# Performance work log

Hardware: AMD Instinct MI355X
Metric: run time of the kernel (lower is better)

The kernel has to match this reference:

```python
import jax, jax.numpy as jnp
import numpy as np

NUM_EMBEDDINGS = 1024
EMBEDDING_DIM = 64


def setup_inputs() -> dict:
    key = jax.random.key(0)
    k1, k2 = jax.random.split(key)
    x = jax.random.normal(k1, (32, 64, 32, 32), dtype=jnp.float32)
    # embeddings initialized uniform(-1/K, 1/K) as in the torch module
    codebook = jax.random.uniform(
        k2, (NUM_EMBEDDINGS, EMBEDDING_DIM), dtype=jnp.float32,
        minval=-1.0 / NUM_EMBEDDINGS, maxval=1.0 / NUM_EMBEDDINGS)
    return {"x": x, "codebook": codebook}


def reference(x, codebook):
    # x: [B, D, H, W] -> [B, H, W, D]
    xp = jnp.transpose(x, (0, 2, 3, 1))
    B, H, W, D = xp.shape
    K = codebook.shape[0]
    xf = xp.reshape(-1, D)  # [N, D]
    # squared L2 distances via expansion (argmin identical to torch.norm argmin)
    x2 = jnp.sum(xf * xf, axis=1, keepdims=True)          # [N, 1]
    c2 = jnp.sum(codebook * codebook, axis=1)             # [K]
    d2 = x2 - 2.0 * (xf @ codebook.T) + c2[None, :]       # [N, K]
    idx = jnp.argmin(d2, axis=1)                          # [N]
    encodings = jax.nn.one_hot(idx, K, dtype=jnp.float32)  # [N, K]
    quantized = codebook[idx]                             # [N, D] == encodings @ codebook
    quantized = quantized.reshape(B, H, W, D).transpose(0, 3, 1, 2)
    return encodings, quantized
```

## Files before the change

### kernel.cpp

```cpp
#include <hip/hip_runtime.h>

#define N_PIX   32768
#define DIM     64
#define K_CODES 1024
#define NCHUNK  4
#define CHUNK   (K_CODES / NCHUNK)


__global__ __launch_bounds__(256) void c2_kernel(const float* __restrict__ cb,
                                                 float* __restrict__ c2) {
    int k = blockIdx.x * 256 + threadIdx.x;
    if (k >= K_CODES) return;
    const float* row = cb + k * DIM;
    float a0 = 0.f, a1 = 0.f, a2 = 0.f, a3 = 0.f;
#pragma unroll
    for (int d = 0; d < DIM; d += 4) {
        a0 = fmaf(row[d + 0], row[d + 0], a0);
        a1 = fmaf(row[d + 1], row[d + 1], a1);
        a2 = fmaf(row[d + 2], row[d + 2], a2);
        a3 = fmaf(row[d + 3], row[d + 3], a3);
    }
    c2[k] = (a0 + a1) + (a2 + a3);
}

__global__ __launch_bounds__(256, 2) void argmin_lds(const float* __restrict__ x,
                                                     const float* __restrict__ cb,
                                                     const float* __restrict__ c2,
                                                     float2* __restrict__ part) {
    __shared__ alignas(16) float4 lds_cb[CHUNK * (DIM / 4)];
    __shared__ float lds_c2[CHUNK];

    int blk    = blockIdx.x;
    int pixblk = blk >> 2;
    int chunk  = blk & 3;
    int t  = threadIdx.x;
    int k0 = chunk * CHUNK;

    {
        const float4* cb4 = reinterpret_cast<const float4*>(cb) + (size_t)k0 * (DIM / 4);
#pragma unroll
        for (int i = 0; i < 16; ++i)
            lds_cb[t + i * 256] = cb4[t + i * 256];
        lds_c2[t] = c2[k0 + t];
    }

    int p  = pixblk * 256 + t;
    int bb = p >> 10;
    int hw = p & 1023;

    const float* xb = x + (size_t)bb * (DIM * 1024) + hw;
#define LDX(i) make_float4(xb[(size_t)(4*(i)+0) << 10], xb[(size_t)(4*(i)+1) << 10], \
                           xb[(size_t)(4*(i)+2) << 10], xb[(size_t)(4*(i)+3) << 10])
    float4 x0 = LDX(0),  x1 = LDX(1),  x2v = LDX(2),  x3 = LDX(3);
    float4 x4 = LDX(4),  x5 = LDX(5),  x6 = LDX(6),   x7 = LDX(7);
    float4 x8 = LDX(8),  x9 = LDX(9),  x10 = LDX(10), x11 = LDX(11);
    float4 x12 = LDX(12), x13 = LDX(13), x14 = LDX(14), x15 = LDX(15);
#undef LDX

    float s0 = 0.f, s1 = 0.f, s2 = 0.f, s3 = 0.f;
#define SQ(v) { s0 = fmaf(v.x, v.x, s0); s1 = fmaf(v.y, v.y, s1); \
                s2 = fmaf(v.z, v.z, s2); s3 = fmaf(v.w, v.w, s3); }
    SQ(x0) SQ(x1) SQ(x2v) SQ(x3) SQ(x4) SQ(x5) SQ(x6) SQ(x7)
    SQ(x8) SQ(x9) SQ(x10) SQ(x11) SQ(x12) SQ(x13) SQ(x14) SQ(x15)
#undef SQ
    float x2 = (s0 + s1) + (s2 + s3);

    __syncthreads();

#define PIN(v) asm volatile("" : "+v"(v.x), "+v"(v.y), "+v"(v.z), "+v"(v.w));
    PIN(x0) PIN(x1) PIN(x2v) PIN(x3) PIN(x4) PIN(x5) PIN(x6) PIN(x7)
    PIN(x8) PIN(x9) PIN(x10) PIN(x11) PIN(x12) PIN(x13) PIN(x14) PIN(x15)
#undef PIN

    float best = 1e30f;
    int   bidx = 0;
    for (int kk = 0; kk < CHUNK; ++kk) {
        const float4* wrow = &lds_cb[kk * (DIM / 4)];
        float c2k = lds_c2[kk];
        float a0 = 0.f, a1 = 0.f, a2 = 0.f, a3 = 0.f;
#define STEP(i, xi) { float4 w = wrow[i]; \
        a0 = fmaf(xi.x, w.x, a0); a1 = fmaf(xi.y, w.y, a1); \
        a2 = fmaf(xi.z, w.z, a2); a3 = fmaf(xi.w, w.w, a3); }
        STEP(0, x0)  STEP(1, x1)  STEP(2, x2v)  STEP(3, x3)
        STEP(4, x4)  STEP(5, x5)  STEP(6, x6)   STEP(7, x7)
        STEP(8, x8)  STEP(9, x9)  STEP(10, x10) STEP(11, x11)
        STEP(12, x12) STEP(13, x13) STEP(14, x14) STEP(15, x15)
#undef STEP
        float dot = (a0 + a1) + (a2 + a3);
        float u    = x2 - 2.0f * dot;
        float dist = u + c2k;
        if (dist < best) { best = dist; bidx = k0 + kk; }
    }
    float2 r;
    r.x = best;
    r.y = __int_as_float(bidx);
    part[(size_t)chunk * N_PIX + p] = r;
}

__global__ __launch_bounds__(128) void reduce_quant(const float* __restrict__ cb,
                                                    const float2* __restrict__ part,
                                                    int* __restrict__ idx,
                                                    float* __restrict__ quant) {
    int n = blockIdx.x * 128 + threadIdx.x;
    float best = 1e30f;
    int   bi = 0;
#pragma unroll
    for (int c = 0; c < NCHUNK; ++c) {
        float2 r = part[(size_t)c * N_PIX + n];
        if (r.x < best) { best = r.x; bi = __float_as_int(r.y); }
    }
    idx[n] = bi;

    int bb = n >> 10;
    int hw = n & 1023;
    const float4* crow = reinterpret_cast<const float4*>(cb + (size_t)bi * DIM);
    float* qb = quant + (size_t)bb * (DIM * 1024) + hw;
#pragma unroll
    for (int dq = 0; dq < 16; ++dq) {
        float4 cv = crow[dq];
        qb[(size_t)(dq * 4 + 0) << 10] = cv.x;
        qb[(size_t)(dq * 4 + 1) << 10] = cv.y;
        qb[(size_t)(dq * 4 + 2) << 10] = cv.z;
        qb[(size_t)(dq * 4 + 3) << 10] = cv.w;
    }
}

__global__ __launch_bounds__(256) void enc_write(const int* __restrict__ idx,
                                                 float* __restrict__ enc) {
    const int TOT = (N_PIX / 4) * K_CODES;
    int tid = blockIdx.x * 256 + threadIdx.x;
    float4* enc4 = reinterpret_cast<float4*>(enc);
    for (int e = tid; e < TOT; e += 2048 * 256) {
        int n  = e >> 8;
        int j0 = (e & 255) << 2;
        int ir = idx[n];
        float4 v;
        v.x = (ir == j0 + 0) ? 1.0f : 0.0f;
        v.y = (ir == j0 + 1) ? 1.0f : 0.0f;
        v.z = (ir == j0 + 2) ? 1.0f : 0.0f;
        v.w = (ir == j0 + 3) ? 1.0f : 0.0f;
        enc4[e] = v;
    }
}

extern "C" void kernel_launch(void* const* d_in, const int* in_sizes, int n_in,
                              void* d_out, int out_size, void* d_ws, size_t ws_size,
                              hipStream_t stream) {
    const float* x  = (const float*)d_in[0];
    const float* cb = (const float*)d_in[1];

    float*  c2   = (float*)d_ws;
    float2* part = (float2*)((char*)d_ws + 4096);
    int*    idx  = (int*)((char*)d_ws + 4096 + (size_t)NCHUNK * N_PIX * 8);

    float* enc   = (float*)d_out;
    float* quant = (float*)d_out + (size_t)N_PIX * K_CODES;

    c2_kernel<<<K_CODES / 256, 256, 0, stream>>>(cb, c2);
    argmin_lds<<<(N_PIX / 256) * NCHUNK, 256, 0, stream>>>(x, cb, c2, part);
    reduce_quant<<<N_PIX / 128, 128, 0, stream>>>(cb, part, idx, quant);
    enc_write<<<2048, 256, 0, stream>>>(idx, enc);
}
```

Baseline: 255.4 us.

## Register-block four pixels per thread in argmin and split codebook into eight chunks

Each thread now holds four pixels' 64-dim vectors in registers, so every codebook row read from LDS is reused across four dot products instead of one. To keep the grid size up, the codebook is split into eight chunks of 128 codes rather than four, and the grid becomes 32 pixel blocks times 8 chunks. This cuts LDS read traffic per FMA, but needs about 256 VGPRs for the x values plus accumulators, so launch bounds drop to one block per CU. That risks lower occupancy or spills, and the partial-results buffer and reduce kernel now handle twice as many chunks.

```diff
diff --git a/kernel.cpp b/kernel.cpp
--- a/kernel.cpp
+++ b/kernel.cpp
@@ -3,7 +3,7 @@
 #define N_PIX   32768
 #define DIM     64
 #define K_CODES 1024
-#define NCHUNK  4
+#define NCHUNK  8
 #define CHUNK   (K_CODES / NCHUNK)
 
 
@@ -23,7 +23,7 @@
     c2[k] = (a0 + a1) + (a2 + a3);
 }
 
-__global__ __launch_bounds__(256, 2) void argmin_lds(const float* __restrict__ x,
+__global__ __launch_bounds__(256, 1) void argmin_lds(const float* __restrict__ x,
                                                      const float* __restrict__ cb,
                                                      const float* __restrict__ c2,
                                                      float2* __restrict__ part) {
@@ -31,70 +31,103 @@
     __shared__ float lds_c2[CHUNK];
 
     int blk    = blockIdx.x;
-    int pixblk = blk >> 2;
-    int chunk  = blk & 3;
+    int pixblk = blk >> 3;
+    int chunk  = blk & 7;
     int t  = threadIdx.x;
     int k0 = chunk * CHUNK;
 
     {
         const float4* cb4 = reinterpret_cast<const float4*>(cb) + (size_t)k0 * (DIM / 4);
 #pragma unroll
-        for (int i = 0; i < 16; ++i)
+        for (int i = 0; i < 8; ++i)
             lds_cb[t + i * 256] = cb4[t + i * 256];
-        lds_c2[t] = c2[k0 + t];
+        if (t < CHUNK) lds_c2[t] = c2[k0 + t];
     }
 
-    int p  = pixblk * 256 + t;
-    int bb = p >> 10;
-    int hw = p & 1023;
+    const float* xb0 = x + (size_t)pixblk * (DIM * 1024) + t;
+    const float* xb1 = xb0 + 256;
+    const float* xb2 = xb0 + 512;
+    const float* xb3 = xb0 + 768;
 
-    const float* xb = x + (size_t)bb * (DIM * 1024) + hw;
-#define LDX(i) make_float4(xb[(size_t)(4*(i)+0) << 10], xb[(size_t)(4*(i)+1) << 10], \
-                           xb[(size_t)(4*(i)+2) << 10], xb[(size_t)(4*(i)+3) << 10])
-    float4 x0 = LDX(0),  x1 = LDX(1),  x2v = LDX(2),  x3 = LDX(3);
-    float4 x4 = LDX(4),  x5 = LDX(5),  x6 = LDX(6),   x7 = LDX(7);
-    float4 x8 = LDX(8),  x9 = LDX(9),  x10 = LDX(10), x11 = LDX(11);
-    float4 x12 = LDX(12), x13 = LDX(13), x14 = LDX(14), x15 = LDX(15);
+#define LDX(b, i) make_float4(b[(size_t)(4*(i)+0) << 10], b[(size_t)(4*(i)+1) << 10], \
+                              b[(size_t)(4*(i)+2) << 10], b[(size_t)(4*(i)+3) << 10])
+#define DECLX(p, b) \
+    float4 x##p##_0 = LDX(b,0),  x##p##_1 = LDX(b,1),  x##p##_2 = LDX(b,2),  x##p##_3 = LDX(b,3), \
+           x##p##_4 = LDX(b,4),  x##p##_5 = LDX(b,5),  x##p##_6 = LDX(b,6),  x##p##_7 = LDX(b,7), \
+           x##p##_8 = LDX(b,8),  x##p##_9 = LDX(b,9),  x##p##_10 = LDX(b,10), x##p##_11 = LDX(b,11), \
+           x##p##_12 = LDX(b,12), x##p##_13 = LDX(b,13), x##p##_14 = LDX(b,14), x##p##_15 = LDX(b,15);
+    DECLX(0, xb0) DECLX(1, xb1) DECLX(2, xb2) DECLX(3, xb3)
 #undef LDX
+#undef DECLX
 
-    float s0 = 0.f, s1 = 0.f, s2 = 0.f, s3 = 0.f;
 #define SQ(v) { s0 = fmaf(v.x, v.x, s0); s1 = fmaf(v.y, v.y, s1); \
                 s2 = fmaf(v.z, v.z, s2); s3 = fmaf(v.w, v.w, s3); }
-    SQ(x0) SQ(x1) SQ(x2v) SQ(x3) SQ(x4) SQ(x5) SQ(x6) SQ(x7)
-    SQ(x8) SQ(x9) SQ(x10) SQ(x11) SQ(x12) SQ(x13) SQ(x14) SQ(x15)
+#define XNORM(p) float xn##p; { float s0=0.f,s1=0.f,s2=0.f,s3=0.f; \
+    SQ(x##p##_0) SQ(x##p##_1) SQ(x##p##_2) SQ(x##p##_3) \
+    SQ(x##p##_4) SQ(x##p##_5) SQ(x##p##_6) SQ(x##p##_7) \
+    SQ(x##p##_8) SQ(x##p##_9) SQ(x##p##_10) SQ(x##p##_11) \
+    SQ(x##p##_12) SQ(x##p##_13) SQ(x##p##_14) SQ(x##p##_15) \
+    xn##p = (s0 + s1) + (s2 + s3); }
+    XNORM(0) XNORM(1) XNORM(2) XNORM(3)
+#undef XNORM
 #undef SQ
-    float x2 = (s0 + s1) + (s2 + s3);
 
     __syncthreads();
 
 #define PIN(v) asm volatile("" : "+v"(v.x), "+v"(v.y), "+v"(v.z), "+v"(v.w));
-    PIN(x0) PIN(x1) PIN(x2v) PIN(x3) PIN(x4) PIN(x5) PIN(x6) PIN(x7)
-    PIN(x8) PIN(x9) PIN(x10) PIN(x11) PIN(x12) PIN(x13) PIN(x14) PIN(x15)
+#define PINP(p) PIN(x##p##_0) PIN(x##p##_1) PIN(x##p##_2) PIN(x##p##_3) \
+                PIN(x##p##_4) PIN(x##p##_5) PIN(x##p##_6) PIN(x##p##_7) \
+                PIN(x##p##_8) PIN(x##p##_9) PIN(x##p##_10) PIN(x##p##_11) \
+                PIN(x##p##_12) PIN(x##p##_13) PIN(x##p##_14) PIN(x##p##_15)
+    PINP(0) PINP(1) PINP(2) PINP(3)
+#undef PINP
 #undef PIN
 
-    float best = 1e30f;
-    int   bidx = 0;
+    float best0 = 1e30f, best1 = 1e30f, best2 = 1e30f, best3 = 1e30f;
+    int   bi0 = 0, bi1 = 0, bi2 = 0, bi3 = 0;
+
+#define FMA_PIX(p, i, w) \
+    a##p##_0 = fmaf(x##p##_##i.x, w.x, a##p##_0); \
+    a##p##_1 = fmaf(x##p##_##i.y, w.y, a##p##_1); \
+    a##p##_2 = fmaf(x##p##_##i.z, w.z, a##p##_2); \
+    a##p##_3 = fmaf(x##p##_##i.w, w.w, a##p##_3);
+#define STEP(i) { float4 w = wrow[i]; \
+    FMA_PIX(0, i, w) FMA_PIX(1, i, w) FMA_PIX(2, i, w) FMA_PIX(3, i, w) }
+
     for (int kk = 0; kk < CHUNK; ++kk) {
         const float4* wrow = &lds_cb[kk * (DIM / 4)];
         float c2k = lds_c2[kk];
-        float a0 = 0.f, a1 = 0.f, a2 = 0.f, a3 = 0.f;
-#define STEP(i, xi) { float4 w = wrow[i]; \
-        a0 = fmaf(xi.x, w.x, a0); a1 = fmaf(xi.y, w.y, a1); \
-        a2 = fmaf(xi.z, w.z, a2); a3 = fmaf(xi.w, w.w, a3); }
-        STEP(0, x0)  STEP(1, x1)  STEP(2, x2v)  STEP(3, x3)
-        STEP(4, x4)  STEP(5, x5)  STEP(6, x6)   STEP(7, x7)
-        STEP(8, x8)  STEP(9, x9)  STEP(10, x10) STEP(11, x11)
-        STEP(12, x12) STEP(13, x13) STEP(14, x14) STEP(15, x15)
+        float a0_0 = 0.f, a0_1 = 0.f, a0_2 = 0.f, a0_3 = 0.f;
+        float a1_0 = 0.f, a1_1 = 0.f, a1_2 = 0.f, a1_3 = 0.f;
+        float a2_0 = 0.f, a2_1 = 0.f, a2_2 = 0.f, a2_3 = 0.f;
+        float a3_0 = 0.f, a3_1 = 0.f, a3_2 = 0.f, a3_3 = 0.f;
+        STEP(0)  STEP(1)  STEP(2)  STEP(3)
+        STEP(4)  STEP(5)  STEP(6)  STEP(7)
+        STEP(8)  STEP(9)  STEP(10) STEP(11)
+        STEP(12) STEP(13) STEP(14) STEP(15)
+        float dot0 = (a0_0 + a0_1) + (a0_2 + a0_3);
+        float dot1 = (a1_0 + a1_1) + (a1_2 + a1_3);
+        float dot2 = (a2_0 + a2_1) + (a2_2 + a2_3);
+        float dot3 = (a3_0 + a3_1) + (a3_2 + a3_3);
+        float d0 = (xn0 - 2.0f * dot0) + c2k;
+        float d1 = (xn1 - 2.0f * dot1) + c2k;
+        float d2 = (xn2 - 2.0f * dot2) + c2k;
+        float d3 = (xn3 - 2.0f * dot3) + c2k;
+        int k = k0 + kk;
+        if (d0 < best0) { best0 = d0; bi0 = k; }
+        if (d1 < best1) { best1 = d1; bi1 = k; }
+        if (d2 < best2) { best2 = d2; bi2 = k; }
+        if (d3 < best3) { best3 = d3; bi3 = k; }
+    }
 #undef STEP
-        float dot = (a0 + a1) + (a2 + a3);
-        float u    = x2 - 2.0f * dot;
-        float dist = u + c2k;
-        if (dist < best) { best = dist; bidx = k0 + kk; }
-    }
+#undef FMA_PIX
+
+    int p0 = pixblk * 1024 + t;
     float2 r;
-    r.x = best;
-    r.y = __int_as_float(bidx);
-    part[(size_t)chunk * N_PIX + p] = r;
+    r.x = best0; r.y = __int_as_float(bi0); part[(size_t)chunk * N_PIX + p0      ] = r;
+    r.x = best1; r.y = __int_as_float(bi1); part[(size_t)chunk * N_PIX + p0 + 256] = r;
+    r.x = best2; r.y = __int_as_float(bi2); part[(size_t)chunk * N_PIX + p0 + 512] = r;
+    r.x = best3; r.y = __int_as_float(bi3); part[(size_t)chunk * N_PIX + p0 + 768] = r;
 }
 
 __global__ __launch_bounds__(128) void reduce_quant(const float* __restrict__ cb,
@@ -157,7 +190,7 @@
     float* quant = (float*)d_out + (size_t)N_PIX * K_CODES;
 
     c2_kernel<<<K_CODES / 256, 256, 0, stream>>>(cb, c2);
-    argmin_lds<<<(N_PIX / 256) * NCHUNK, 256, 0, stream>>>(x, cb, c2, part);
+    argmin_lds<<<(N_PIX / 1024) * NCHUNK, 256, 0, stream>>>(x, cb, c2, part);
     reduce_quant<<<N_PIX / 128, 128, 0, stream>>>(cb, part, idx, quant);
     enc_write<<<2048, 256, 0, stream>>>(idx, enc);
 }
```

Result: slower. 287.0 us (+12.4%).
